# Optimization experiments

Hardware: AMD Instinct MI355X
Metric: run time of the kernel (lower is better)

## Reference

```python
import jax, jax.numpy as jnp
import numpy as np

N_NODES = 50000
N_EDGES = 800000
IN_DIM = 128
HID = 128
N_GRAPHS = 64


def setup_inputs() -> dict:
    key = jax.random.key(0)
    ks = jax.random.split(key, 12)
    edge_index = jax.random.randint(ks[0], (2, N_EDGES), 0, N_NODES, dtype=jnp.int64)
    edge_weight = jax.random.uniform(ks[1], (N_EDGES,), dtype=jnp.float32)
    input_feature = jax.random.normal(ks[2], (N_NODES, IN_DIM), dtype=jnp.float32)
    graph_indicator = jnp.sort(jax.random.randint(ks[3], (N_NODES,), 0, N_GRAPHS, dtype=jnp.int64))
    s = 0.05
    W1 = jax.random.normal(ks[4], (IN_DIM, HID), dtype=jnp.float32) * s
    b1 = jnp.zeros((HID,), jnp.float32)
    W2 = jax.random.normal(ks[5], (HID, HID), dtype=jnp.float32) * s
    b2 = jnp.zeros((HID,), jnp.float32)
    W3 = jax.random.normal(ks[6], (HID, HID), dtype=jnp.float32) * s
    b3 = jnp.zeros((HID,), jnp.float32)
    wa = jax.random.normal(ks[7], (3 * HID, 1), dtype=jnp.float32) * s
    ba = jnp.zeros((1,), jnp.float32)
    Wf = jax.random.normal(ks[8], (3 * HID * 2, IN_DIM), dtype=jnp.float32) * s
    bf = jnp.zeros((IN_DIM,), jnp.float32)
    return dict(edge_index=edge_index, edge_weight=edge_weight,
                input_feature=input_feature, graph_indicator=graph_indicator,
                W1=W1, b1=b1, W2=W2, b2=b2, W3=W3, b3=b3,
                wa=wa, ba=ba, Wf=Wf, bf=bf)


def reference(edge_index, edge_weight, input_feature, graph_indicator,
              W1, b1, W2, b2, W3, b3, wa, ba, Wf, bf):
    src, dst = edge_index[0], edge_index[1]

    def gcn(x, W, b):
        # GraphConvolution: adj @ (x @ W) + b, adj given as weighted edge list
        support = x @ W  # [N, d_out]
        msg = edge_weight[:, None] * support[src]  # [E, d_out] gather
        return jax.ops.segment_sum(msg, dst, num_segments=N_NODES) + b

    g1 = jax.nn.relu(gcn(input_feature, W1, b1))
    g2 = jax.nn.relu(gcn(g1, W2, b2))
    g3 = jax.nn.relu(gcn(g2, W3, b3))
    h = jnp.concatenate([g1, g2, g3], axis=1)  # [N, 3*HID]

    # SelfAttentionPooling: attention score via a 1-dim GraphConvolution, tanh gate
    score = jnp.tanh(gcn(h, wa, ba))  # [N, 1]
    pool = h * score

    # segment avg / max pooling per graph
    seg_sum = jax.ops.segment_sum(pool, graph_indicator, num_segments=N_GRAPHS)
    counts = jax.ops.segment_sum(jnp.ones((N_NODES, 1), pool.dtype), graph_indicator,
                                 num_segments=N_GRAPHS)
    avg = seg_sum / jnp.maximum(counts, 1.0)
    mx = jax.ops.segment_max(pool, graph_indicator, num_segments=N_GRAPHS)
    pooled = jnp.concatenate([avg, mx], axis=1)  # [G, 6*HID]

    return jax.nn.relu(pooled @ Wf + bf)  # [G, IN_DIM]
```

## Files before the change

kernel.cpp:

```cpp
#include <hip/hip_runtime.h>
#include <math.h>

#define HID 128
#define POOL_SEG 16
#define WT_STRIDE 136
#define ELL_D 48
#define SC_CHUNK 2048
#define FXS 16384.0f
#define FXI (1.0f/16384.0f)
#define FG_KC 12

typedef __attribute__((ext_vector_type(8))) short short8;
typedef __attribute__((ext_vector_type(4))) float float4v;

__device__ inline short f2bf(float f) {
  unsigned u = __builtin_bit_cast(unsigned, f);
  unsigned r = (u + 0x7fff + ((u >> 16) & 1)) >> 16;
  return (short)r;
}
__device__ inline unsigned pack2bf(float lo, float hi) {
  return (unsigned)(unsigned short)f2bf(lo) | ((unsigned)(unsigned short)f2bf(hi) << 16);
}
__device__ inline float bflo(unsigned u) { return __builtin_bit_cast(float, u << 16); }
__device__ inline float bfhi(unsigned u) { return __builtin_bit_cast(float, u & 0xffff0000u); }
__device__ inline float bf2f(unsigned short s) { return __builtin_bit_cast(float, (unsigned)s << 16); }
__device__ inline unsigned short f2h(float f) {
  _Float16 h = (_Float16)f;
  return __builtin_bit_cast(unsigned short, h);
}
__device__ inline float h2f(unsigned short hb) {
  return (float)__builtin_bit_cast(_Float16, hb);
}

__global__ void detect_flags(const int* __restrict__ ei, const int* __restrict__ gi,
                             int* __restrict__ flags, int n_nodes) {
  if (blockIdx.x == 0 && threadIdx.x == 0) {
    int nz = 0;
    for (int i = 1; i < 64; i += 2) nz |= ei[i];
    flags[0] = (nz == 0) ? 1 : 0;
    flags[1] = (gi[n_nodes - 1] == 0) ? 1 : 0;
  }
}

__global__ void prep_edges(const void* __restrict__ ei_raw, const int* __restrict__ flags,
                           const float* __restrict__ ew, int2* __restrict__ packed, int E) {
  int e = blockIdx.x * blockDim.x + threadIdx.x;
  if (e >= E) return;
  int s, d;
  if (flags[0]) {
    const long long* p = (const long long*)ei_raw;
    s = (int)p[e]; d = (int)p[E + e];
  } else {
    const int* p = (const int*)ei_raw;
    s = p[e]; d = p[E + e];
  }
  packed[e] = make_int2((d << 16) | s, __builtin_bit_cast(int, ew[e]));
}

__global__ void scatter_ell(const int2* __restrict__ packed, int* __restrict__ cursor,
                            unsigned* __restrict__ ell, int E, int N) {
  int group = blockIdx.x & 7;
  int chunk = blockIdx.x >> 3;
  int rng = (N + 7) >> 3;
  int lo = group * rng;
  int hi = lo + rng; if (hi > N) hi = N;
  int base = chunk * SC_CHUNK;
  for (int i = 0; i < SC_CHUNK; i += 256) {
    int e = base + i + threadIdx.x;
    if (e < E) {
      int2 rec = packed[e];
      int d = ((unsigned)rec.x) >> 16;
      if (d >= lo && d < hi) {
        unsigned s = (unsigned)rec.x & 0xFFFFu;
        unsigned short wh = f2h(__builtin_bit_cast(float, rec.y));
        int pos = atomicAdd(&cursor[d], 1);
        if (pos < ELL_D)
          ell[(size_t)d * ELL_D + pos] = (s << 16) | (unsigned)wh;
      }
    }
  }
}

__global__ void convert_w(const float* __restrict__ W1, const float* __restrict__ W2,
                          const float* __restrict__ W3, short* __restrict__ T1,
                          short* __restrict__ T2, short* __restrict__ T3) {
  int i = blockIdx.x * blockDim.x + threadIdx.x;
  int which = i >> 14, idx = i & 16383;
  int k = idx >> 7, n = idx & 127;
  const float* W = (which == 0) ? W1 : ((which == 1) ? W2 : W3);
  short* T = (which == 0) ? T1 : ((which == 1) ? T2 : T3);
  T[n * WT_STRIDE + k] = f2bf(W[idx]);
}

__global__ __launch_bounds__(256) void gemm_mfma(const float* __restrict__ Af,
                                                 const unsigned short* __restrict__ Abf,
                                                 const short* __restrict__ Wt,
                                                 unsigned short* __restrict__ C,
                                                 int n, int a_is_bf16) {
  __shared__ short Wlds[128 * WT_STRIDE];
  int t = threadIdx.x;
  {
    const ulonglong2* gsrc = (const ulonglong2*)Wt;
    ulonglong2* ldst = (ulonglong2*)Wlds;
    for (int i = t; i < (128 * WT_STRIDE) / 8; i += 256) ldst[i] = gsrc[i];
  }
  __syncthreads();

  int wave = t >> 6, lane = t & 63;
  int quad = lane >> 4, l15 = lane & 15;
  int m0 = blockIdx.x * 64 + wave * 16;

  int m = m0 + l15; if (m >= n) m = n - 1;
  short8 afrag[4];
  if (a_is_bf16) {
    const unsigned short* Arow = Abf + (size_t)m * 128;
#pragma unroll
    for (int c = 0; c < 4; c++) afrag[c] = *(const short8*)(Arow + c * 32 + quad * 8);
  } else {
    const float* Arow = Af + (size_t)m * 128;
#pragma unroll
    for (int c = 0; c < 4; c++) {
      int k0 = c * 32 + quad * 8;
      float4 x = *(const float4*)(Arow + k0);
      float4 y = *(const float4*)(Arow + k0 + 4);
      short8 a;
      a[0] = f2bf(x.x); a[1] = f2bf(x.y); a[2] = f2bf(x.z); a[3] = f2bf(x.w);
      a[4] = f2bf(y.x); a[5] = f2bf(y.y); a[6] = f2bf(y.z); a[7] = f2bf(y.w);
      afrag[c] = a;
    }
  }

  float4v acc[8];
#pragma unroll
  for (int tt = 0; tt < 8; tt++) acc[tt] = (float4v){0.f, 0.f, 0.f, 0.f};

#pragma unroll
  for (int c = 0; c < 4; c++) {
    int kb = c * 32 + quad * 8;
#pragma unroll
    for (int tt = 0; tt < 8; tt++) {
      const short8* bp = (const short8*)&Wlds[(tt * 16 + l15) * WT_STRIDE + kb];
      acc[tt] = __builtin_amdgcn_mfma_f32_16x16x32_bf16(afrag[c], *bp, acc[tt], 0, 0, 0);
    }
  }

  int rbase = m0 + quad * 4;
#pragma unroll
  for (int tt = 0; tt < 8; tt++) {
    int col = tt * 16 + l15;
#pragma unroll
    for (int r = 0; r < 4; r++) {
      int row = rbase + r;
      if (row < n) C[(size_t)row * 128 + col] = (unsigned short)f2bf(acc[tt][r]);
    }
  }
}

__global__ void aggregate(const unsigned short* __restrict__ support,
                          const int* __restrict__ deg_arr,
                          const unsigned* __restrict__ ell,
                          const float* __restrict__ bias, unsigned short* __restrict__ out,
                          const unsigned short* __restrict__ g1p,
                          const unsigned short* __restrict__ g2p,
                          const float* __restrict__ wa,
                          float* __restrict__ s_pre,
                          int n, int do_score) {
  int gid = blockIdx.x * blockDim.x + threadIdx.x;
  int node = gid >> 4, q = gid & 15;
  if (node >= n) return;
  int deg = deg_arr[node]; if (deg > ELL_D) deg = ELL_D;
  const unsigned* row = ell + (size_t)node * ELL_D;
  int acc[8];
#pragma unroll
  for (int j = 0; j < 8; j++) acc[j] = 0;
  const uint4* s4 = (const uint4*)support;

  int i = 0;
  for (; i + 3 < deg; i += 4) {
    unsigned r0 = row[i], r1 = row[i + 1], r2 = row[i + 2], r3 = row[i + 3];
    float w0 = h2f((unsigned short)(r0 & 0xFFFF)) * FXS;
    float w1 = h2f((unsigned short)(r1 & 0xFFFF)) * FXS;
    float w2 = h2f((unsigned short)(r2 & 0xFFFF)) * FXS;
    float w3 = h2f((unsigned short)(r3 & 0xFFFF)) * FXS;
    uint4 v0 = s4[(size_t)(r0 >> 16) * 16 + q];
    uint4 v1 = s4[(size_t)(r1 >> 16) * 16 + q];
    uint4 v2 = s4[(size_t)(r2 >> 16) * 16 + q];
    uint4 v3 = s4[(size_t)(r3 >> 16) * 16 + q];
    acc[0] += __float2int_rn(w0 * bflo(v0.x)); acc[1] += __float2int_rn(w0 * bfhi(v0.x));
    acc[2] += __float2int_rn(w0 * bflo(v0.y)); acc[3] += __float2int_rn(w0 * bfhi(v0.y));
    acc[4] += __float2int_rn(w0 * bflo(v0.z)); acc[5] += __float2int_rn(w0 * bfhi(v0.z));
    acc[6] += __float2int_rn(w0 * bflo(v0.w)); acc[7] += __float2int_rn(w0 * bfhi(v0.w));
    acc[0] += __float2int_rn(w1 * bflo(v1.x)); acc[1] += __float2int_rn(w1 * bfhi(v1.x));
    acc[2] += __float2int_rn(w1 * bflo(v1.y)); acc[3] += __float2int_rn(w1 * bfhi(v1.y));
    acc[4] += __float2int_rn(w1 * bflo(v1.z)); acc[5] += __float2int_rn(w1 * bfhi(v1.z));
    acc[6] += __float2int_rn(w1 * bflo(v1.w)); acc[7] += __float2int_rn(w1 * bfhi(v1.w));
    acc[0] += __float2int_rn(w2 * bflo(v2.x)); acc[1] += __float2int_rn(w2 * bfhi(v2.x));
    acc[2] += __float2int_rn(w2 * bflo(v2.y)); acc[3] += __float2int_rn(w2 * bfhi(v2.y));
    acc[4] += __float2int_rn(w2 * bflo(v2.z)); acc[5] += __float2int_rn(w2 * bfhi(v2.z));
    acc[6] += __float2int_rn(w2 * bflo(v2.w)); acc[7] += __float2int_rn(w2 * bfhi(v2.w));
    acc[0] += __float2int_rn(w3 * bflo(v3.x)); acc[1] += __float2int_rn(w3 * bfhi(v3.x));
    acc[2] += __float2int_rn(w3 * bflo(v3.y)); acc[3] += __float2int_rn(w3 * bfhi(v3.y));
    acc[4] += __float2int_rn(w3 * bflo(v3.z)); acc[5] += __float2int_rn(w3 * bfhi(v3.z));
    acc[6] += __float2int_rn(w3 * bflo(v3.w)); acc[7] += __float2int_rn(w3 * bfhi(v3.w));
  }
  for (; i < deg; i++) {
    unsigned r0 = row[i];
    float w0 = h2f((unsigned short)(r0 & 0xFFFF)) * FXS;
    uint4 v0 = s4[(size_t)(r0 >> 16) * 16 + q];
    acc[0] += __float2int_rn(w0 * bflo(v0.x)); acc[1] += __float2int_rn(w0 * bfhi(v0.x));
    acc[2] += __float2int_rn(w0 * bflo(v0.y)); acc[3] += __float2int_rn(w0 * bfhi(v0.y));
    acc[4] += __float2int_rn(w0 * bflo(v0.z)); acc[5] += __float2int_rn(w0 * bfhi(v0.z));
    acc[6] += __float2int_rn(w0 * bflo(v0.w)); acc[7] += __float2int_rn(w0 * bfhi(v0.w));
  }

  float f[8];
#pragma unroll
  for (int j = 0; j < 8; j++) f[j] = (float)acc[j] * FXI;

  float4 b0 = ((const float4*)bias)[q * 2];
  float4 b1 = ((const float4*)bias)[q * 2 + 1];
  f[0] = fmaxf(f[0] + b0.x, 0.f); f[1] = fmaxf(f[1] + b0.y, 0.f);
  f[2] = fmaxf(f[2] + b0.z, 0.f); f[3] = fmaxf(f[3] + b0.w, 0.f);
  f[4] = fmaxf(f[4] + b1.x, 0.f); f[5] = fmaxf(f[5] + b1.y, 0.f);
  f[6] = fmaxf(f[6] + b1.z, 0.f); f[7] = fmaxf(f[7] + b1.w, 0.f);

  uint4 o;
  o.x = pack2bf(f[0], f[1]); o.y = pack2bf(f[2], f[3]);
  o.z = pack2bf(f[4], f[5]); o.w = pack2bf(f[6], f[7]);
  ((uint4*)out)[(size_t)node * 16 + q] = o;

  if (do_score) {
    int d0 = q * 8;
    uint4 u1 = ((const uint4*)g1p)[(size_t)node * 16 + q];
    uint4 u2 = ((const uint4*)g2p)[(size_t)node * 16 + q];
    const float* wa1 = wa + d0;
    const float* wa2 = wa + 128 + d0;
    const float* wa3 = wa + 256 + d0;
    float sc = bflo(u1.x) * wa1[0] + bfhi(u1.x) * wa1[1]
             + bflo(u1.y) * wa1[2] + bfhi(u1.y) * wa1[3]
             + bflo(u1.z) * wa1[4] + bfhi(u1.z) * wa1[5]
             + bflo(u1.w) * wa1[6] + bfhi(u1.w) * wa1[7]
             + bflo(u2.x) * wa2[0] + bfhi(u2.x) * wa2[1]
             + bflo(u2.y) * wa2[2] + bfhi(u2.y) * wa2[3]
             + bflo(u2.z) * wa2[4] + bfhi(u2.z) * wa2[5]
             + bflo(u2.w) * wa2[6] + bfhi(u2.w) * wa2[7];
#pragma unroll
    for (int j = 0; j < 8; j++) sc += f[j] * wa3[j];
#pragma unroll
    for (int m = 1; m < 16; m <<= 1) sc += __shfl_xor(sc, m, 64);
    if (q == 0) s_pre[node] = sc;
  }
}

__global__ void att_aggregate(const float* __restrict__ s_pre, const int* __restrict__ deg_arr,
                              const unsigned* __restrict__ ell,
                              const float* __restrict__ ba, float* __restrict__ score, int n) {
  int node = blockIdx.x * blockDim.x + threadIdx.x;
  if (node >= n) return;
  int deg = deg_arr[node]; if (deg > ELL_D) deg = ELL_D;
  const unsigned* row = ell + (size_t)node * ELL_D;
  int acc = 0;
  for (int i = 0; i < deg; i++) {
    unsigned r = row[i];
    acc += __float2int_rn(h2f((unsigned short)(r & 0xFFFF)) * FXS * s_pre[r >> 16]);
  }
  score[node] = tanhf((float)acc * FXI + ba[0]);
}

__global__ void graph_bounds(const void* __restrict__ gi_raw, const int* __restrict__ flags,
                             int* __restrict__ gstart, int n, int ngraphs) {
  int g = threadIdx.x;
  if (g > ngraphs) return;
  if (g == ngraphs) { gstart[g] = n; return; }
  bool is64 = flags[1] != 0;
  const long long* g64 = (const long long*)gi_raw;
  const int* g32 = (const int*)gi_raw;
  int lo = 0, hi = n;
  while (lo < hi) {
    int mid = (lo + hi) >> 1;
    long long v = is64 ? g64[mid] : (long long)g32[mid];
    if (v < (long long)g) lo = mid + 1; else hi = mid;
  }
  gstart[g] = lo;
}

__global__ __launch_bounds__(384) void pool_partial(const unsigned short* __restrict__ g1,
                                                    const unsigned short* __restrict__ g2,
                                                    const unsigned short* __restrict__ g3,
                                                    const float* __restrict__ score,
                                                    const int* __restrict__ gstart,
                                                    float* __restrict__ part) {
  int g = blockIdx.x / POOL_SEG, seg = blockIdx.x % POOL_SEG;
  int d = threadIdx.x;
  int sg = d >> 7, dd = d & 127;
  const unsigned short* gp = (sg == 0) ? g1 : ((sg == 1) ? g2 : g3);
  int s = gstart[g], e = gstart[g + 1];
  int len = e - s;
  int chunk = (len + POOL_SEG - 1) / POOL_SEG;
  int ns = s + seg * chunk;
  int ne = ns + chunk; if (ne > e) ne = e;
  float sum = 0.f, mx = -3.402823466e38f;
  for (int node = ns; node < ne; node++) {
    float sc = score[node];
    float v = bf2f(gp[(size_t)node * 128 + dd]) * sc;
    sum += v;
    mx = fmaxf(mx, v);
  }
  size_t base = (size_t)blockIdx.x * 768;
  part[base + d] = sum;
  part[base + 384 + d] = mx;
}

__global__ __launch_bounds__(384) void pool_combine(const float* __restrict__ part,
                                                    const int* __restrict__ gstart,
                                                    float* __restrict__ pooled) {
  int g = blockIdx.x;
  int d = threadIdx.x;
  float sum = 0.f, mx = -3.402823466e38f;
  for (int seg = 0; seg < POOL_SEG; seg++) {
    size_t base = ((size_t)g * POOL_SEG + seg) * 768;
    sum += part[base + d];
    mx = fmaxf(mx, part[base + 384 + d]);
  }
  float cnt = (float)(gstart[g + 1] - gstart[g]);
  pooled[(size_t)g * 768 + d] = sum / fmaxf(cnt, 1.0f);
  pooled[(size_t)g * 768 + 384 + d] = mx;
}

__global__ __launch_bounds__(128) void fg_partial(const float* __restrict__ pooled,
                                                  const float* __restrict__ Wf,
                                                  float* __restrict__ fgp) {
  int g = blockIdx.x / FG_KC, kc = blockIdx.x % FG_KC;
  int c = threadIdx.x;
  __shared__ float row[64];
  if (c < 64) row[c] = pooled[(size_t)g * 768 + kc * 64 + c];
  __syncthreads();
  const float* Wp = Wf + (size_t)kc * 64 * 128 + c;
  float acc = 0.f;
#pragma unroll 8
  for (int k = 0; k < 64; k++) acc += row[k] * Wp[k * 128];
  fgp[((size_t)g * FG_KC + kc) * 128 + c] = acc;
}

__global__ __launch_bounds__(128) void fg_combine(const float* __restrict__ fgp,
                                                  const float* __restrict__ bf,
                                                  float* __restrict__ out) {
  int g = blockIdx.x;
  int c = threadIdx.x;
  float acc = bf[c];
#pragma unroll
  for (int kc = 0; kc < FG_KC; kc++)
    acc += fgp[((size_t)g * FG_KC + kc) * 128 + c];
  out[(size_t)g * 128 + c] = fmaxf(acc, 0.f);
}

extern "C" void kernel_launch(void* const* d_in, const int* in_sizes, int n_in,
                              void* d_out, int out_size, void* d_ws, size_t ws_size,
                              hipStream_t stream) {
  const void* ei_raw = d_in[0];
  const float* ew    = (const float*)d_in[1];
  const float* X     = (const float*)d_in[2];
  const void* gi_raw = d_in[3];
  const float* W1 = (const float*)d_in[4];  const float* b1 = (const float*)d_in[5];
  const float* W2 = (const float*)d_in[6];  const float* b2 = (const float*)d_in[7];
  const float* W3 = (const float*)d_in[8];  const float* b3 = (const float*)d_in[9];
  const float* wa = (const float*)d_in[10]; const float* ba = (const float*)d_in[11];
  const float* Wf = (const float*)d_in[12]; const float* bf = (const float*)d_in[13];
  float* out = (float*)d_out;

  const int E = in_sizes[1];
  const int N = in_sizes[2] / 128;
  const int G = out_size / 128;

  char* ws = (char*)d_ws;
  size_t off = 0;
  auto take = [&](size_t bytes) {
    char* p = ws + off;
    off = (off + bytes + 255) & ~(size_t)255;
    return p;
  };
  int*      flags   = (int*)take(16);
  int*      cursor  = (int*)take((size_t)N * 4);
  int2*     packed  = (int2*)take((size_t)E * 8);
  unsigned* ell     = (unsigned*)take((size_t)N * ELL_D * 4);
  short*    wt1     = (short*)take((size_t)128 * WT_STRIDE * 2);
  short*    wt2     = (short*)take((size_t)128 * WT_STRIDE * 2);
  short*    wt3     = (short*)take((size_t)128 * WT_STRIDE * 2);
  unsigned short* support = (unsigned short*)take((size_t)N * 128 * 2);
  unsigned short* g1      = (unsigned short*)take((size_t)N * 128 * 2);
  unsigned short* g2      = (unsigned short*)take((size_t)N * 128 * 2);
  unsigned short* g3      = (unsigned short*)take((size_t)N * 128 * 2);
  float* s_pre   = (float*)take((size_t)N * 4);
  float* score   = (float*)take((size_t)N * 4);
  int*   gstart  = (int*)take((size_t)(G + 1) * 4);
  float* part    = (float*)take((size_t)G * POOL_SEG * 768 * 4);
  float* pooled  = (float*)take((size_t)G * 768 * 4);
  float* fgp     = (float*)take((size_t)G * FG_KC * 128 * 4);
  if (off > ws_size) return;

  hipMemsetAsync(cursor, 0, (size_t)N * 4, stream);
  detect_flags<<<1, 64, 0, stream>>>((const int*)ei_raw, (const int*)gi_raw, flags, N);
  prep_edges<<<(E + 255) / 256, 256, 0, stream>>>(ei_raw, flags, ew, packed, E);
  convert_w<<<(3 * 16384 + 255) / 256, 256, 0, stream>>>(W1, W2, W3, wt1, wt2, wt3);
  {
    int chunks = (E + SC_CHUNK - 1) / SC_CHUNK;
    scatter_ell<<<8 * chunks, 256, 0, stream>>>(packed, cursor, ell, E, N);
  }

  const int GB = (N + 63) / 64;
  const int AB = (N * 16 + 255) / 256;
  gemm_mfma<<<GB, 256, 0, stream>>>(X, (const unsigned short*)nullptr, wt1, support, N, 0);
  aggregate<<<AB, 256, 0, stream>>>(support, cursor, ell, b1, g1,
                                    nullptr, nullptr, nullptr, nullptr, N, 0);
  gemm_mfma<<<GB, 256, 0, stream>>>((const float*)nullptr, g1, wt2, support, N, 1);
  aggregate<<<AB, 256, 0, stream>>>(support, cursor, ell, b2, g2,
                                    nullptr, nullptr, nullptr, nullptr, N, 0);
  gemm_mfma<<<GB, 256, 0, stream>>>((const float*)nullptr, g2, wt3, support, N, 1);
  aggregate<<<AB, 256, 0, stream>>>(support, cursor, ell, b3, g3,
                                    g1, g2, wa, s_pre, N, 1);

  att_aggregate<<<(N + 255) / 256, 256, 0, stream>>>(s_pre, cursor, ell, ba, score, N);

  graph_bounds<<<1, 128, 0, stream>>>(gi_raw, flags, gstart, N, G);
  pool_partial<<<G * POOL_SEG, 384, 0, stream>>>(g1, g2, g3, score, gstart, part);
  pool_combine<<<G, 384, 0, stream>>>(part, gstart, pooled);
  fg_partial<<<G * FG_KC, 128, 0, stream>>>(pooled, Wf, fgp);
  fg_combine<<<G, 128, 0, stream>>>(fgp, bf, out);
}
```

Before: 323.5 us.

## Pre-bin edges by destination group before ELL scatter

Replaces the edge packing kernel and the 8-way filtered scatter with a binning pass. Edges are bucketed into 8 destination-range groups using block-local counts and one global atomic per group, so each scatter block reads only the edges of its own group instead of re-reading all edges and discarding seven eighths. The binned buffer is sized 8*E, which adds workspace, and the binning pass adds shared-memory atomics and scattered writes. The encoding keeps 13 bits for the local destination index.

After: 326.5 us. Within noise of the previous version (+1.0%).

```diff
diff --git a/kernel.cpp b/kernel.cpp
--- a/kernel.cpp
+++ b/kernel.cpp
@@ -9,6 +9,9 @@
 #define FXS 16384.0f
 #define FXI (1.0f/16384.0f)
 #define FG_KC 12
+#define BIN_TPB 256
+#define BIN_EPT 16
+#define BIN_EPB (BIN_TPB * BIN_EPT)
 
 typedef __attribute__((ext_vector_type(8))) short short8;
 typedef __attribute__((ext_vector_type(4))) float float4v;
@@ -42,41 +45,70 @@
   }
 }
 
-__global__ void prep_edges(const void* __restrict__ ei_raw, const int* __restrict__ flags,
-                           const float* __restrict__ ew, int2* __restrict__ packed, int E) {
-  int e = blockIdx.x * blockDim.x + threadIdx.x;
-  if (e >= E) return;
-  int s, d;
-  if (flags[0]) {
-    const long long* p = (const long long*)ei_raw;
-    s = (int)p[e]; d = (int)p[E + e];
-  } else {
-    const int* p = (const int*)ei_raw;
-    s = p[e]; d = p[E + e];
-  }
-  packed[e] = make_int2((d << 16) | s, __builtin_bit_cast(int, ew[e]));
-}
-
-__global__ void scatter_ell(const int2* __restrict__ packed, int* __restrict__ cursor,
-                            unsigned* __restrict__ ell, int E, int N) {
+__global__ __launch_bounds__(BIN_TPB) void bin_edges(const void* __restrict__ ei_raw,
+                                                     const int* __restrict__ flags,
+                                                     const float* __restrict__ ew,
+                                                     int* __restrict__ gcur,
+                                                     int2* __restrict__ binned, int E, int N) {
+  __shared__ int cnt[8], base_s[8], loc[8];
+  int t = threadIdx.x;
+  if (t < 8) { cnt[t] = 0; loc[t] = 0; }
+  __syncthreads();
+  int rng = (N + 7) >> 3;
+  bool is64 = flags[0] != 0;
+  const long long* p64 = (const long long*)ei_raw;
+  const int* p32 = (const int*)ei_raw;
+  unsigned pk[BIN_EPT];
+  float wv[BIN_EPT];
+  int base = blockIdx.x * BIN_EPB;
+#pragma unroll
+  for (int j = 0; j < BIN_EPT; j++) {
+    int e = base + j * BIN_TPB + t;
+    pk[j] = 0xFFFFFFFFu;
+    if (e < E) {
+      int s = is64 ? (int)p64[e] : p32[e];
+      int d = is64 ? (int)p64[E + e] : p32[E + e];
+      int g = d / rng;
+      pk[j] = ((unsigned)g << 29) | ((unsigned)(d - g * rng) << 16) | (unsigned)s;
+      wv[j] = ew[e];
+      atomicAdd(&cnt[g], 1);
+    }
+  }
+  __syncthreads();
+  if (t < 8) base_s[t] = atomicAdd(&gcur[t], cnt[t]);
+  __syncthreads();
+#pragma unroll
+  for (int j = 0; j < BIN_EPT; j++) {
+    if (pk[j] != 0xFFFFFFFFu) {
+      int g = pk[j] >> 29;
+      int pos = atomicAdd(&loc[g], 1);
+      binned[(size_t)g * E + base_s[g] + pos] =
+          make_int2((int)pk[j], __builtin_bit_cast(int, wv[j]));
+    }
+  }
+}
+
+__global__ void scatter_ell2(const int2* __restrict__ binned, const int* __restrict__ gcnt,
+                             int* __restrict__ cursor, unsigned* __restrict__ ell,
+                             int E, int N) {
   int group = blockIdx.x & 7;
   int chunk = blockIdx.x >> 3;
+  int cnt = gcnt[group];
+  int base = chunk * SC_CHUNK;
+  if (base >= cnt) return;
   int rng = (N + 7) >> 3;
   int lo = group * rng;
-  int hi = lo + rng; if (hi > N) hi = N;
-  int base = chunk * SC_CHUNK;
+  const int2* src = binned + (size_t)group * E;
   for (int i = 0; i < SC_CHUNK; i += 256) {
-    int e = base + i + threadIdx.x;
-    if (e < E) {
-      int2 rec = packed[e];
-      int d = ((unsigned)rec.x) >> 16;
-      if (d >= lo && d < hi) {
-        unsigned s = (unsigned)rec.x & 0xFFFFu;
-        unsigned short wh = f2h(__builtin_bit_cast(float, rec.y));
-        int pos = atomicAdd(&cursor[d], 1);
-        if (pos < ELL_D)
-          ell[(size_t)d * ELL_D + pos] = (s << 16) | (unsigned)wh;
-      }
+    int idx = base + i + threadIdx.x;
+    if (idx < cnt) {
+      int2 rec = src[idx];
+      int d = lo + (((unsigned)rec.x >> 16) & 0x1FFFu);
+      unsigned s = (unsigned)rec.x & 0xFFFFu;
+      unsigned short wh = f2h(__builtin_bit_cast(float, rec.y));
+      int pos = atomicAdd(&cursor[d], 1);
+      if (pos < ELL_D)
+        ell[(size_t)d * ELL_D + pos] = (s << 16) | (unsigned)wh;
     }
   }
 }
@@ -380,8 +412,9 @@
     return p;
   };
   int*      flags   = (int*)take(16);
-  int*      cursor  = (int*)take((size_t)N * 4);
-  int2*     packed  = (int2*)take((size_t)E * 8);
+  int*      cursor  = (int*)take((size_t)(N + 8) * 4);
+  int*      gcur    = cursor + N;
+  int2*     binned  = (int2*)take((size_t)8 * E * 8);
   unsigned* ell     = (unsigned*)take((size_t)N * ELL_D * 4);
   short*    wt1     = (short*)take((size_t)128 * WT_STRIDE * 2);
   short*    wt2     = (short*)take((size_t)128 * WT_STRIDE * 2);
@@ -398,13 +431,14 @@
   float* fgp     = (float*)take((size_t)G * FG_KC * 128 * 4);
   if (off > ws_size) return;
 
-  hipMemsetAsync(cursor, 0, (size_t)N * 4, stream);
+  hipMemsetAsync(cursor, 0, (size_t)(N + 8) * 4, stream);
   detect_flags<<<1, 64, 0, stream>>>((const int*)ei_raw, (const int*)gi_raw, flags, N);
-  prep_edges<<<(E + 255) / 256, 256, 0, stream>>>(ei_raw, flags, ew, packed, E);
   convert_w<<<(3 * 16384 + 255) / 256, 256, 0, stream>>>(W1, W2, W3, wt1, wt2, wt3);
+  bin_edges<<<(E + BIN_EPB - 1) / BIN_EPB, BIN_TPB, 0, stream>>>(ei_raw, flags, ew,
+                                                                 gcur, binned, E, N);
   {
     int chunks = (E + SC_CHUNK - 1) / SC_CHUNK;
-    scatter_ell<<<8 * chunks, 256, 0, stream>>>(packed, cursor, ell, E, N);
+    scatter_ell2<<<8 * chunks, 256, 0, stream>>>(binned, gcur, cursor, ell, E, N);
   }
 
   const int GB = (N + 63) / 64;
```
